# Kernel tuning notes

Measured on AMD Instinct MI355X. Metric: run time of the kernel, lower is better.

The kernel has to match this reference:

```python
import jax, jax.numpy as jnp
import numpy as np

B, S, I, E, D = 64, 512, 64, 256, 256  # batch, src_len, input_size, enc_hid, dec_hid


def _lstm_cell(h, c, x, Wih, Whh, b):
    # PyTorch LSTM gate order: i, f, g, o ; b = b_ih + b_hh combined
    z = x @ Wih.T + h @ Whh.T + b
    i, f, g, o = jnp.split(z, 4, axis=-1)
    c = jax.nn.sigmoid(f) * c + jax.nn.sigmoid(i) * jnp.tanh(g)
    h = jax.nn.sigmoid(o) * jnp.tanh(c)
    return h, c


def _run_lstm(x, h0, c0, Wih, Whh, b):
    # x: [B,S,I] -> outputs [B,S,H]
    def step(carry, xt):
        h, c = _lstm_cell(carry[0], carry[1], xt, Wih, Whh, b)
        return (h, c), h
    _, ys = jax.lax.scan(step, (h0, c0), jnp.swapaxes(x, 0, 1))
    return jnp.swapaxes(ys, 0, 1)


def _forward(x, enc_h0, enc_c0, dec_h0, dec_c0, Wih_f, Whh_f, b_f, Wih_b, Whh_b, b_b,
             W_attn, b_attn, v, Wih_d, Whh_d, b_d, W_lin, b_lin):
    b_, s_ = x.shape[0], x.shape[1]
    # bidirectional encoder
    out_f = _run_lstm(x, enc_h0[0], enc_c0[0], Wih_f, Whh_f, b_f)
    out_b = _run_lstm(x[:, ::-1, :], enc_h0[1], enc_c0[1], Wih_b, Whh_b, b_b)[:, ::-1, :]
    enc_out = jnp.concatenate([out_f, out_b], axis=-1)  # [B,S,2E]
    h0d, c0d = dec_h0[0], dec_c0[0]  # decoder re-starts from these EVERY step (faithful)

    @jax.checkpoint
    def dec_step(carry, _):
        y, h_attn = carry  # y: [B,1], h_attn: [B,D]
        dh = h_attn.shape[-1]
        cat = jnp.concatenate(
            [jnp.broadcast_to(h_attn[:, None, :], (b_, s_, dh)), enc_out], axis=-1)
        energy = jnp.tanh(cat @ W_attn.T + b_attn)              # [B,S,D]
        attn = jax.nn.softmax(jnp.einsum('d,bsd->bs', v, energy), axis=1)
        context = jnp.einsum('bs,bse->be', attn, enc_out)       # [B,2E]
        dec_in = jnp.concatenate([y, context], axis=-1)         # [B,1+2E]
        h_new, _c = _lstm_cell(h0d, c0d, dec_in, Wih_d, Whh_d, b_d)
        y_new = jnp.concatenate([h_new, context], axis=-1) @ W_lin.T + b_lin  # [B,1]
        return (y_new, h_new), y_new

    y0 = jnp.zeros((b_, 1), dtype=x.dtype)
    _, ys = jax.lax.scan(dec_step, (y0, h0d), None, length=s_)  # [S,B,1]
    # output_size == 1, so torch's cat-then-[:,1:] equals the stacked per-step ys
    return jnp.swapaxes(ys, 0, 1).reshape(b_, s_)


def setup_inputs() -> dict:
    key = jax.random.key(0)
    ks = jax.random.split(key, 20)
    W = 0.05  # weight scale ~ torch default init magnitude
    rn = lambda k, sh, s: jax.random.normal(k, sh, dtype=jnp.float32) * s
    return {
        'x': rn(ks[0], (B, S, I), 1.0),
        'enc_h0': rn(ks[1], (2, B, E), 1.0),
        'enc_c0': rn(ks[2], (2, B, E), 1.0),
        'dec_h0': rn(ks[3], (1, B, D), 1.0),
        'dec_c0': rn(ks[4], (1, B, D), 1.0),
        'Wih_f': rn(ks[5], (4 * E, I), W),
        'Whh_f': rn(ks[6], (4 * E, E), W),
        'b_f': rn(ks[7], (4 * E,), W),
        'Wih_b': rn(ks[8], (4 * E, I), W),
        'Whh_b': rn(ks[9], (4 * E, E), W),
        'b_b': rn(ks[10], (4 * E,), W),
        'W_attn': rn(ks[11], (D, D + 2 * E), W),
        'b_attn': rn(ks[12], (D,), W),
        'v': jax.random.uniform(ks[13], (D,), dtype=jnp.float32),
        'Wih_d': rn(ks[14], (4 * D, 2 * E + 1), W),
        'Whh_d': rn(ks[15], (4 * D, D), W),
        'b_d': rn(ks[16], (4 * D,), W),
        'W_lin': rn(ks[17], (1, 2 * E + D), W),
        'b_lin': rn(ks[18], (1,), W),
    }


def reference(x, enc_h0, enc_c0, dec_h0, dec_c0, Wih_f, Whh_f, b_f, Wih_b, Whh_b, b_b,
              W_attn, b_attn, v, Wih_d, Whh_d, b_d, W_lin, b_lin):
    return _forward(x, enc_h0, enc_c0, dec_h0, dec_c0, Wih_f, Whh_f, b_f,
                    Wih_b, Whh_b, b_b, W_attn, b_attn, v, Wih_d, Whh_d, b_d,
                    W_lin, b_lin)
```

## Files before the change

### kernel.cpp

```cpp
#include <hip/hip_runtime.h>
#include <hip/hip_bf16.h>

#define NB 64
#define NS 512
#define NI 64
#define NE 256
#define ND 256
#define N4E 1024
#define N4D 1024
#define NTE 512
#define G 4
#define SLICE 128
#define CELLS 64

__device__ __forceinline__ float fsig(float x){
    return __fdividef(1.f, 1.f + __expf(-x));
}
__device__ __forceinline__ float ftanh(float x){
    x = fminf(10.f, fmaxf(-10.f, x));
    float e = __expf(2.f*x);
    return 1.f - __fdividef(2.f, e + 1.f);
}
__device__ __forceinline__ float wave_sum(float v){
    #pragma unroll
    for (int o=32;o>0;o>>=1) v += __shfl_xor(v, o, 64);
    return v;
}
__device__ __forceinline__ float wave_max(float v){
    #pragma unroll
    for (int o=32;o>0;o>>=1) v = fmaxf(v, __shfl_xor(v, o, 64));
    return v;
}
__device__ __forceinline__ float blo(unsigned u){ return __uint_as_float(u<<16); }
__device__ __forceinline__ float bhi(unsigned u){ return __uint_as_float(u & 0xffff0000u); }
__device__ __forceinline__ unsigned short bfbits(float f){
    __hip_bfloat16 h = __float2bfloat16(f);
    return *(unsigned short*)&h;
}
__device__ __forceinline__ float ld_agf(const float* p){
    return __hip_atomic_load(p, __ATOMIC_RELAXED, __HIP_MEMORY_SCOPE_AGENT);
}
__device__ __forceinline__ void st_agf(float* p, float v){
    __hip_atomic_store(p, v, __ATOMIC_RELAXED, __HIP_MEMORY_SCOPE_AGENT);
}

__device__ __forceinline__ void groupbar(unsigned* c, unsigned tgt, int tid){
    __syncthreads();
    if (tid == 0){
        __hip_atomic_fetch_add(c, 1u, __ATOMIC_RELAXED, __HIP_MEMORY_SCOPE_AGENT);
        while (__hip_atomic_load(c, __ATOMIC_RELAXED, __HIP_MEMORY_SCOPE_AGENT) < tgt)
            __builtin_amdgcn_s_sleep(2);
    }
    __syncthreads();
}

__global__ void k_transpose(float* __restrict__ dst, const float* __restrict__ src,
                            int R, int C, int ld, int off){
    int idx = blockIdx.x*256 + threadIdx.x;
    if (idx >= R*C) return;
    int r = idx / C, c = idx - r*C;
    dst[(size_t)c*R + r] = src[(size_t)r*ld + off + c];
}
__global__ void k_transpose16(__hip_bfloat16* __restrict__ dst, const float* __restrict__ src,
                              int R, int C, int ld, int off){
    int idx = blockIdx.x*256 + threadIdx.x;
    if (idx >= R*C) return;
    int r = idx / C, c = idx - r*C;
    dst[(size_t)c*R + r] = __float2bfloat16(src[(size_t)r*ld + off + c]);
}

__global__ void k_pack_wy(float* __restrict__ wy, const float* __restrict__ Wih_d){
    int j = blockIdx.x*256 + threadIdx.x;
    if (j < N4D) wy[j] = Wih_d[(size_t)j*(NTE+1)];
}

__global__ void k_pack_wdtg(__hip_bfloat16* __restrict__ dst, const float* __restrict__ Wih_d){
    int idx = blockIdx.x*256 + threadIdx.x;
    int q = idx >> 17, rem = idx & 131071;
    int e = rem >> 8, jj = rem & 255;
    int j = ((jj>>6)<<8) + (q<<6) + (jj&63);
    dst[idx] = __float2bfloat16(Wih_d[(size_t)j*(NTE+1) + 1 + e]);
}

__global__ void k_zc(float* __restrict__ zc, const float* __restrict__ WhhTd,
                     const float* __restrict__ h0d, const float* __restrict__ b_d){
    int b = blockIdx.x, tid = threadIdx.x;
    __shared__ float h0[ND];
    if (tid < ND) h0[tid] = h0d[b*ND + tid];
    __syncthreads();
    for (int j = tid; j < N4D; j += 256){
        float acc = b_d[j];
        #pragma unroll 8
        for (int d=0; d<ND; ++d) acc = fmaf(h0[d], WhhTd[d*N4D + j], acc);
        zc[b*N4D + j] = acc;
    }
}

__global__ void k_dec_init(float* __restrict__ hG, float* __restrict__ yG,
                           unsigned* __restrict__ ctr, const float* __restrict__ dec_h0){
    int b = blockIdx.x, tid = threadIdx.x;
    hG[b*ND + tid] = dec_h0[b*ND + tid];
    if (tid < G) yG[b*G + tid] = 0.f;
    if (tid == 0) ctr[b] = 0u;
}

__global__ __launch_bounds__(512) void k_enc(
    const float* __restrict__ x, const float* __restrict__ eh0, const float* __restrict__ ec0,
    const __hip_bfloat16* __restrict__ WihTf, const __hip_bfloat16* __restrict__ WhhTf, const float* __restrict__ bf,
    const __hip_bfloat16* __restrict__ WihTb, const __hip_bfloat16* __restrict__ WhhTb, const float* __restrict__ bb,
    __hip_bfloat16* __restrict__ eo16)
{
    int bid = blockIdx.x;
    int dir = bid & 1, b = bid >> 1;
    const unsigned* Wih2 = (const unsigned*)(dir ? WihTb : WihTf);
    const unsigned* Whh2 = (const unsigned*)(dir ? WhhTb : WhhTf);
    const float*  bias = dir ? bb : bf;
    int tid = threadIdx.x;
    __shared__ float h[NE], c[NE], xt[NI], z[N4E];
    __shared__ float2 bl[512];
    bl[tid] = ((const float2*)bias)[tid];
    if (tid < NE){
        h[tid] = eh0[(dir*NB + b)*NE + tid];
        c[tid] = ec0[(dir*NB + b)*NE + tid];
    }
    __syncthreads();
    for (int t=0; t<NS; ++t){
        int st = dir ? (NS-1-t) : t;
        if (tid < NI) xt[tid] = x[((size_t)b*NS + st)*NI + tid];
        __syncthreads();
        float2 acc = bl[tid];
        #pragma unroll 8
        for (int i=0;i<NI;++i){
            float xv = xt[i]; unsigned w = Wih2[i*512 + tid];
            acc.x = fmaf(xv, blo(w), acc.x); acc.y = fmaf(xv, bhi(w), acc.y);
        }
        #pragma unroll 8
        for (int d=0;d<NE;++d){
            float hv = h[d]; unsigned w = Whh2[d*512 + tid];
            acc.x = fmaf(hv, blo(w), acc.x); acc.y = fmaf(hv, bhi(w), acc.y);
        }
        ((float2*)z)[tid] = acc;
        __syncthreads();
        if (tid < NE){
            float zi=z[tid], zf=z[NE+tid], zg=z[2*NE+tid], zo=z[3*NE+tid];
            float cn = fsig(zf)*c[tid] + fsig(zi)*ftanh(zg);
            float hn = fsig(zo)*ftanh(cn);
            c[tid]=cn; h[tid]=hn;
            eo16[((size_t)b*NS + st)*NTE + dir*NE + tid] = __float2bfloat16(hn);
        }
        __syncthreads();
    }
}

__global__ __launch_bounds__(256) void k_encproj(const unsigned* __restrict__ eo32,
        const float* __restrict__ WeT, const float* __restrict__ b_attn,
        unsigned short* __restrict__ ep_pk16){
    int b = blockIdx.y, s0 = blockIdx.x*16, tid = threadIdx.x;
    __shared__ float tile[16*NTE];
    {
        const unsigned* eop = eo32 + (size_t)(b*NS + s0)*256;
        for (int k=0;k<32;++k){
            int wi = k*256 + tid;
            unsigned w = eop[wi];
            int sl = wi>>8, ew = wi&255;
            tile[sl*NTE + 2*ew]   = blo(w);
            tile[sl*NTE + 2*ew+1] = bhi(w);
        }
    }
    __syncthreads();
    float acc[16];
    float ba = b_attn[tid];
    #pragma unroll
    for (int sl=0;sl<16;++sl) acc[sl]=ba;
    #pragma unroll 4
    for (int e4=0;e4<128;++e4){
        float w0 = WeT[(4*e4+0)*ND+tid];
        float w1 = WeT[(4*e4+1)*ND+tid];
        float w2 = WeT[(4*e4+2)*ND+tid];
        float w3 = WeT[(4*e4+3)*ND+tid];
        #pragma unroll
        for (int sl=0;sl<16;++sl){
            const float4 tv = *(const float4*)&tile[sl*NTE + 4*e4];
            acc[sl] = fmaf(tv.x,w0,fmaf(tv.y,w1,fmaf(tv.z,w2,fmaf(tv.w,w3,acc[sl]))));
        }
    }
    #pragma unroll
    for (int sl=0;sl<16;++sl){
        int s = s0+sl;
        size_t wdi = ((size_t)(b*4 + (s>>7))*128 + (tid>>1))*128 + (s&127);
        ep_pk16[wdi*2 + (tid&1)] = bfbits(acc[sl]);
    }
}

__global__ __launch_bounds__(1024, 4) void k_dec(
    const unsigned* __restrict__ eo32,
    const unsigned* __restrict__ ep_pk,
    const unsigned* __restrict__ WhTp,
    const float* __restrict__ v,
    const float* __restrict__ zc, const float* __restrict__ wy,
    const unsigned* __restrict__ WdTp_all,
    const float* __restrict__ dec_c0,
    const float* __restrict__ W_lin, const float* __restrict__ b_lin,
    float* __restrict__ hG, float* __restrict__ yG,
    float* __restrict__ ctxG, float* __restrict__ msG,
    unsigned* __restrict__ ctr,
    float* __restrict__ out)
{
    int bid = blockIdx.x;
    int b = bid & 63, q = bid >> 6;
    int tid = threadIdx.x;

    __shared__ unsigned ep_lds[16384];
    __shared__ float part[2048];
    __shared__ float h_l[ND];
    __shared__ float2 hv[ND];
    __shared__ float v_l[ND];
    __shared__ float scores_l[SLICE];
    __shared__ float ctx_l[NTE];
    __shared__ float z_l[256], zc_l[256], wy_l[256];
    __shared__ float c0_l[CELLS], wlh_l[CELLS], wlc_l[SLICE];
    __shared__ float msbuf[8];
    __shared__ float wred[16];
    __shared__ float smax, yprev;

    const unsigned* WdTp = WdTp_all + (size_t)q*NTE*128;

    for (int i=tid; i<16384; i+=1024)
        ep_lds[i] = ep_pk[(size_t)(b*4+q)*16384 + i];
    unsigned eo_reg[32];
    {
        int ep2 = tid & 255, sq = tid >> 8;
        const unsigned* eop = eo32 + (size_t)(b*NS + q*SLICE + sq*32)*256 + ep2;
        #pragma unroll
        for (int ss=0; ss<32; ++ss) eo_reg[ss] = eop[(size_t)ss*256];
    }
    if (tid < 256){
        int jj = tid;
        int j = ((jj>>6)<<8) + (q<<6) + (jj&63);
        zc_l[jj] = zc[b*N4D + j];
        wy_l[jj] = wy[j];
        v_l[tid] = v[tid];
    }
    if (tid < CELLS){
        c0_l[tid]  = dec_c0[b*ND + q*CELLS + tid];
        wlh_l[tid] = W_lin[q*CELLS + tid];
    }
    if (tid < SLICE) wlc_l[tid] = W_lin[ND + q*SLICE + tid];
    float blin = b_lin[0];
    __syncthreads();

    for (int t=0; t<NS; ++t){
        if (tid < ND) h_l[tid] = ld_agf(&hG[b*ND + tid]);
        if (tid == 0){
            float y = 0.f;
            if (t > 0){
                y = blin + ld_agf(&yG[b*G+0]) + ld_agf(&yG[b*G+1])
                         + ld_agf(&yG[b*G+2]) + ld_agf(&yG[b*G+3]);
                if (q == 0) out[(size_t)b*NS + (t-1)] = y;
            }
            yprev = y;
        }
        __syncthreads();
        {
            int d2 = tid & 127, kq = tid >> 7;
            float ax = 0.f, ay = 0.f;
            #pragma unroll 8
            for (int kk=0; kk<32; ++kk){
                int k = kq*32 + kk;
                unsigned w = WhTp[k*128 + d2];
                float hvv = h_l[k];
                ax = fmaf(hvv, blo(w), ax); ay = fmaf(hvv, bhi(w), ay);
            }
            ((float2*)part)[kq*128 + d2] = make_float2(ax, ay);
        }
        __syncthreads();
        if (tid < ND){
            float s = 0.f;
            #pragma unroll
            for (int r=0;r<8;++r) s += part[r*256 + tid];
            hv[tid] = make_float2(v_l[tid], s);
        }
        __syncthreads();
        {
            int sl = tid & 127, dg = tid >> 7;
            float sc = 0.f;
            const unsigned* epl = ep_lds + dg*16*128 + sl;
            #pragma unroll
            for (int k16=0; k16<16; ++k16){
                unsigned w = epl[k16*128];
                int d = dg*32 + 2*k16;
                float2 a0 = hv[d], a1 = hv[d+1];
                sc += a0.x*ftanh(blo(w) + a0.y) + a1.x*ftanh(bhi(w) + a1.y);
            }
            part[dg*128 + sl] = sc;
        }
        __syncthreads();
        if (tid < SLICE){
            float s = 0.f;
            #pragma unroll
            for (int r=0;r<8;++r) s += part[r*128 + tid];
            part[1024 + tid] = s;
            float wm = wave_max(s);
            if ((tid&63)==0) wred[tid>>6] = wm;
        }
        __syncthreads();
        if (tid == 0) smax = fmaxf(wred[0], wred[1]);
        __syncthreads();
        if (tid < SLICE){
            float ev = __expf(part[1024 + tid] - smax);
            scores_l[tid] = ev;
            float s = wave_sum(ev);
            if ((tid&63)==0) wred[2+(tid>>6)] = s;
        }
        __syncthreads();
        if (tid == 0){
            st_agf(&msG[(b*G+q)*2+0], smax);
            st_agf(&msG[(b*G+q)*2+1], wred[2]+wred[3]);
        }
        {
            int ep2 = tid & 255, sq = tid >> 8;
            float ax = 0.f, ay = 0.f;
            #pragma unroll
            for (int ss=0; ss<32; ++ss){
                unsigned w = eo_reg[ss];
                float sc = scores_l[sq*32 + ss];
                ax = fmaf(sc, blo(w), ax); ay = fmaf(sc, bhi(w), ay);
            }
            ((float2*)part)[sq*256 + ep2] = make_float2(ax, ay);
        }
        __syncthreads();
        if (tid < NTE){
            float s = part[tid] + part[512+tid] + part[1024+tid] + part[1536+tid];
            st_agf(&ctxG[(size_t)(b*G+q)*NTE + tid], s);
        }
        groupbar(&ctr[b], (unsigned)(t*2*G + G), tid);
        if (tid < 2*G) msbuf[tid] = ld_agf(&msG[b*G*2 + tid]);
        __syncthreads();
        float mm = fmaxf(fmaxf(msbuf[0], msbuf[2]), fmaxf(msbuf[4], msbuf[6]));
        float w0 = __expf(msbuf[0]-mm), w1 = __expf(msbuf[2]-mm),
              w2 = __expf(msbuf[4]-mm), w3 = __expf(msbuf[6]-mm);
        float inv = __fdividef(1.f, msbuf[1]*w0 + msbuf[3]*w1 + msbuf[5]*w2 + msbuf[7]*w3);
        if (tid < NTE){
            const float* cg = ctxG + (size_t)b*G*NTE + tid;
            float cacc = ld_agf(cg)*w0 + ld_agf(cg+NTE)*w1
                       + ld_agf(cg+2*NTE)*w2 + ld_agf(cg+3*NTE)*w3;
            ctx_l[tid] = cacc * inv;
        }
        __syncthreads();
        {
            int jj2 = tid & 127, eq = tid >> 7;
            float ax = 0.f, ay = 0.f;
            #pragma unroll 8
            for (int ee=0; ee<64; ++ee){
                int e = eq*64 + ee;
                unsigned w = WdTp[e*128 + jj2];
                float cv = ctx_l[e];
                ax = fmaf(cv, blo(w), ax); ay = fmaf(cv, bhi(w), ay);
            }
            ((float2*)part)[eq*128 + jj2] = make_float2(ax, ay);
        }
        __syncthreads();
        if (tid < 256){
            float s = zc_l[tid] + yprev*wy_l[tid];
            #pragma unroll
            for (int r=0;r<8;++r) s += part[r*256 + tid];
            z_l[tid] = s;
        }
        __syncthreads();
        float yp = 0.f;
        if (tid < CELLS){
            float zi=z_l[tid], zf=z_l[64+tid], zg=z_l[128+tid], zo=z_l[192+tid];
            float cn = fsig(zf)*c0_l[tid] + fsig(zi)*ftanh(zg);
            float hn = fsig(zo)*ftanh(cn);
            st_agf(&hG[b*ND + q*CELLS + tid], hn);
            yp = hn * wlh_l[tid];
        } else if (tid < CELLS + SLICE){
            yp = ctx_l[q*SLICE + (tid - CELLS)] * wlc_l[tid - CELLS];
        }
        {
            float s = wave_sum(yp);
            if ((tid&63)==0 && tid < 192) wred[8+(tid>>6)] = s;
        }
        __syncthreads();
        if (tid == 0) st_agf(&yG[b*G + q], wred[8]+wred[9]+wred[10]);
        groupbar(&ctr[b], (unsigned)(t*2*G + 2*G), tid);
    }
    if (q == 0 && tid == 0){
        out[(size_t)b*NS + (NS-1)] = blin + ld_agf(&yG[b*G+0]) + ld_agf(&yG[b*G+1])
                                          + ld_agf(&yG[b*G+2]) + ld_agf(&yG[b*G+3]);
    }
}

extern "C" void kernel_launch(void* const* d_in, const int* in_sizes, int n_in,
                              void* d_out, int out_size, void* d_ws, size_t ws_size,
                              hipStream_t stream){
    const float* x      = (const float*)d_in[0];
    const float* enc_h0 = (const float*)d_in[1];
    const float* enc_c0 = (const float*)d_in[2];
    const float* dec_h0 = (const float*)d_in[3];
    const float* dec_c0 = (const float*)d_in[4];
    const float* Wih_f  = (const float*)d_in[5];
    const float* Whh_f  = (const float*)d_in[6];
    const float* b_f    = (const float*)d_in[7];
    const float* Wih_b  = (const float*)d_in[8];
    const float* Whh_b  = (const float*)d_in[9];
    const float* b_b    = (const float*)d_in[10];
    const float* W_attn = (const float*)d_in[11];
    const float* b_attn = (const float*)d_in[12];
    const float* v      = (const float*)d_in[13];
    const float* Wih_d  = (const float*)d_in[14];
    const float* Whh_d  = (const float*)d_in[15];
    const float* b_d    = (const float*)d_in[16];
    const float* W_lin  = (const float*)d_in[17];
    const float* b_lin  = (const float*)d_in[18];
    float* out = (float*)d_out;
    char* ws   = (char*)d_ws;

    size_t off = 0;
    auto alloc = [&](size_t bytes)->size_t{ size_t o = off; off += (bytes + 255) & ~(size_t)255; return o; };
    size_t o_eo16   = alloc((size_t)NB*NS*NTE*2);
    size_t o_eppk   = alloc((size_t)NB*G*128*128*4);
    size_t o_WihTf  = alloc((size_t)NI*N4E*2);
    size_t o_WhhTf  = alloc((size_t)NE*N4E*2);
    size_t o_WihTb  = alloc((size_t)NI*N4E*2);
    size_t o_WhhTb  = alloc((size_t)NE*N4E*2);
    size_t o_WhT16  = alloc((size_t)ND*ND*2);
    size_t o_WeT    = alloc((size_t)NTE*ND*4);
    size_t o_WdTg   = alloc((size_t)G*NTE*256*2);
    size_t o_WhhTd  = alloc((size_t)ND*N4D*4);
    size_t o_zc     = alloc((size_t)NB*N4D*4);
    size_t o_wy     = alloc((size_t)N4D*4);
    size_t o_hG     = alloc((size_t)NB*ND*4);
    size_t o_yG     = alloc((size_t)NB*G*4);
    size_t o_ctxG   = alloc((size_t)NB*G*NTE*4);
    size_t o_msG    = alloc((size_t)NB*G*2*4);
    size_t o_ctr    = alloc((size_t)NB*4);
    if (ws_size < off) return;

    auto F   = [&](size_t o)->float*{ return (float*)(ws + o); };
    auto U32 = [&](size_t o)->unsigned*{ return (unsigned*)(ws + o); };
    auto H16 = [&](size_t o)->__hip_bfloat16*{ return (__hip_bfloat16*)(ws + o); };

    auto T32 = [&](size_t dsto, const float* src, int R, int C, int ld, int offc){
        int n = R*C;
        k_transpose<<<dim3((n+255)/256), dim3(256), 0, stream>>>(F(dsto), src, R, C, ld, offc);
    };
    auto T16 = [&](size_t dsto, const float* src, int R, int C, int ld, int offc){
        int n = R*C;
        k_transpose16<<<dim3((n+255)/256), dim3(256), 0, stream>>>(H16(dsto), src, R, C, ld, offc);
    };
    T16(o_WihTf, Wih_f, N4E, NI, NI, 0);
    T16(o_WhhTf, Whh_f, N4E, NE, NE, 0);
    T16(o_WihTb, Wih_b, N4E, NI, NI, 0);
    T16(o_WhhTb, Whh_b, N4E, NE, NE, 0);
    T16(o_WhT16, W_attn, ND, ND, ND+NTE, 0);
    T32(o_WeT,   W_attn, ND, NTE, ND+NTE, ND);
    T32(o_WhhTd, Whh_d, N4D, ND, ND, 0);
    k_pack_wdtg<<<dim3((G*NTE*256)/256), dim3(256), 0, stream>>>(H16(o_WdTg), Wih_d);
    k_pack_wy<<<dim3(4), dim3(256), 0, stream>>>(F(o_wy), Wih_d);
    k_zc<<<dim3(NB), dim3(256), 0, stream>>>(F(o_zc), F(o_WhhTd), dec_h0, b_d);
    k_dec_init<<<dim3(NB), dim3(256), 0, stream>>>(F(o_hG), F(o_yG), (unsigned*)(ws+o_ctr), dec_h0);

    k_enc<<<dim3(2*NB), dim3(512), 0, stream>>>(x, enc_h0, enc_c0,
        H16(o_WihTf), H16(o_WhhTf), b_f, H16(o_WihTb), H16(o_WhhTb), b_b, H16(o_eo16));

    k_encproj<<<dim3(NS/16, NB), dim3(256), 0, stream>>>(U32(o_eo16), F(o_WeT), b_attn,
        (unsigned short*)(ws+o_eppk));

    k_dec<<<dim3(NB*G), dim3(1024), 0, stream>>>(U32(o_eo16), U32(o_eppk),
        U32(o_WhT16), v, F(o_zc), F(o_wy), U32(o_WdTg), dec_c0, W_lin, b_lin,
        F(o_hG), F(o_yG), F(o_ctxG), F(o_msG), (unsigned*)(ws+o_ctr), out);
}
```

Before: 19.51 ms.

## Restructure encoder LSTM to one gate row per thread with packed bf16 weights

Rewrites the encoder LSTM kernel to use 1024 threads per block, one gate row per thread, with row-major bf16-pair packed weights read as uint4. The input-to-hidden weights are held in registers, the x rows are double-buffered and prefetched for the next step, and the cell state stays in registers. Each step loses one barrier and the loads become wide per-row loads instead of strided column reads. In exchange there is more register pressure, and each thread now streams a 512-byte weight row per step whose loads are uncoalesced across the threads of a wave.

```diff
diff --git a/kernel.cpp b/kernel.cpp
--- a/kernel.cpp
+++ b/kernel.cpp
@@ -69,6 +69,15 @@
     dst[(size_t)c*R + r] = __float2bfloat16(src[(size_t)r*ld + off + c]);
 }
 
+__global__ void k_pack_pairs(unsigned* __restrict__ dst, const float* __restrict__ src,
+                             int n, int Cp){
+    int idx = blockIdx.x*256 + threadIdx.x;
+    if (idx >= n) return;
+    int r = idx / Cp, k = idx - r*Cp;
+    const float* s = src + (size_t)r*2*Cp + 2*k;
+    dst[idx] = (unsigned)bfbits(s[0]) | ((unsigned)bfbits(s[1])<<16);
+}
+
 __global__ void k_pack_wy(float* __restrict__ wy, const float* __restrict__ Wih_d){
     int j = blockIdx.x*256 + threadIdx.x;
     if (j < N4D) wy[j] = Wih_d[(size_t)j*(NTE+1)];
@@ -104,49 +113,91 @@
     if (tid == 0) ctr[b] = 0u;
 }
 
-__global__ __launch_bounds__(512) void k_enc(
+__global__ __launch_bounds__(1024, 4) void k_enc(
     const float* __restrict__ x, const float* __restrict__ eh0, const float* __restrict__ ec0,
-    const __hip_bfloat16* __restrict__ WihTf, const __hip_bfloat16* __restrict__ WhhTf, const float* __restrict__ bf,
-    const __hip_bfloat16* __restrict__ WihTb, const __hip_bfloat16* __restrict__ WhhTb, const float* __restrict__ bb,
-    __hip_bfloat16* __restrict__ eo16)
+    const unsigned* __restrict__ whhPKf, const unsigned* __restrict__ wihPKf, const float* __restrict__ bf,
+    const unsigned* __restrict__ whhPKb, const unsigned* __restrict__ wihPKb, const float* __restrict__ bb,
+    unsigned* __restrict__ eo32)
 {
     int bid = blockIdx.x;
-    int dir = bid & 1, b = bid >> 1;
-    const unsigned* Wih2 = (const unsigned*)(dir ? WihTb : WihTf);
-    const unsigned* Whh2 = (const unsigned*)(dir ? WhhTb : WhhTf);
-    const float*  bias = dir ? bb : bf;
+    int b = bid & 63, dir = bid >> 6;
     int tid = threadIdx.x;
-    __shared__ float h[NE], c[NE], xt[NI], z[N4E];
-    __shared__ float2 bl[512];
-    bl[tid] = ((const float2*)bias)[tid];
-    if (tid < NE){
-        h[tid] = eh0[(dir*NB + b)*NE + tid];
-        c[tid] = ec0[(dir*NB + b)*NE + tid];
+    const unsigned* whhPK = dir ? whhPKb : whhPKf;
+    const unsigned* wihPK = dir ? wihPKb : wihPKf;
+    const float* bias = dir ? bb : bf;
+
+    __shared__ __align__(16) float h_l[NE];
+    __shared__ __align__(16) float xt[2][NI];
+    __shared__ float z_l[N4E];
+
+    unsigned wih_r[32];
+    {
+        const uint4* wr = (const uint4*)(wihPK + (size_t)tid*32);
+        #pragma unroll
+        for (int k=0;k<8;++k) ((uint4*)wih_r)[k] = wr[k];
+    }
+    const uint4* wrow = (const uint4*)(whhPK + (size_t)tid*128);
+    float bias_r = bias[tid];
+
+    float c0r=0.f, c1r=0.f;
+    if (tid < 128){
+        h_l[2*tid]   = eh0[(dir*NB+b)*NE + 2*tid];
+        h_l[2*tid+1] = eh0[(dir*NB+b)*NE + 2*tid+1];
+        c0r = ec0[(dir*NB+b)*NE + 2*tid];
+        c1r = ec0[(dir*NB+b)*NE + 2*tid+1];
+    }
+    {
+        int st0 = dir ? (NS-1) : 0;
+        if (tid < 16) ((float4*)xt[0])[tid] = ((const float4*)(x + ((size_t)b*NS+st0)*NI))[tid];
     }
     __syncthreads();
-    for (int t=0; t<NS; ++t){
+
+    for (int t=0;t<NS;++t){
         int st = dir ? (NS-1-t) : t;
-        if (tid < NI) xt[tid] = x[((size_t)b*NS + st)*NI + tid];
-        __syncthreads();
-        float2 acc = bl[tid];
-        #pragma unroll 8
-        for (int i=0;i<NI;++i){
-            float xv = xt[i]; unsigned w = Wih2[i*512 + tid];
-            acc.x = fmaf(xv, blo(w), acc.x); acc.y = fmaf(xv, bhi(w), acc.y);
-        }
-        #pragma unroll 8
-        for (int d=0;d<NE;++d){
-            float hv = h[d]; unsigned w = Whh2[d*512 + tid];
-            acc.x = fmaf(hv, blo(w), acc.x); acc.y = fmaf(hv, bhi(w), acc.y);
-        }
-        ((float2*)z)[tid] = acc;
-        __syncthreads();
-        if (tid < NE){
-            float zi=z[tid], zf=z[NE+tid], zg=z[2*NE+tid], zo=z[3*NE+tid];
-            float cn = fsig(zf)*c[tid] + fsig(zi)*ftanh(zg);
-            float hn = fsig(zo)*ftanh(cn);
-            c[tid]=cn; h[tid]=hn;
-            eo16[((size_t)b*NS + st)*NTE + dir*NE + tid] = __float2bfloat16(hn);
+        float4 xpre = make_float4(0.f,0.f,0.f,0.f);
+        if (t+1 < NS && tid < 16){
+            int stn = dir ? (NS-2-t) : (t+1);
+            xpre = ((const float4*)(x + ((size_t)b*NS+stn)*NI))[tid];
+        }
+        const float* xc = xt[t&1];
+        float a0=bias_r, a1=0.f, a2=0.f, a3=0.f;
+        #pragma unroll
+        for (int k=0;k<16;++k){
+            float4 xv = ((const float4*)xc)[k];
+            unsigned w0 = wih_r[2*k], w1 = wih_r[2*k+1];
+            a0 = fmaf(xv.x, blo(w0), a0);
+            a1 = fmaf(xv.y, bhi(w0), a1);
+            a2 = fmaf(xv.z, blo(w1), a2);
+            a3 = fmaf(xv.w, bhi(w1), a3);
+        }
+        const float4* h4 = (const float4*)h_l;
+        #pragma unroll
+        for (int kk=0;kk<32;++kk){
+            uint4 w = wrow[kk];
+            float4 ha = h4[2*kk], hb = h4[2*kk+1];
+            a0 = fmaf(ha.x, blo(w.x), a0);
+            a1 = fmaf(ha.y, bhi(w.x), a1);
+            a2 = fmaf(ha.z, blo(w.y), a2);
+            a3 = fmaf(ha.w, bhi(w.y), a3);
+            a0 = fmaf(hb.x, blo(w.z), a0);
+            a1 = fmaf(hb.y, bhi(w.z), a1);
+            a2 = fmaf(hb.z, blo(w.w), a2);
+            a3 = fmaf(hb.w, bhi(w.w), a3);
+        }
+        z_l[tid] = (a0+a1)+(a2+a3);
+        if (t+1 < NS && tid < 16) ((float4*)xt[(t+1)&1])[tid] = xpre;
+        __syncthreads();
+        if (tid < 128){
+            int d0 = 2*tid, d1 = 2*tid+1;
+            float zi0=z_l[d0], zf0=z_l[NE+d0], zg0=z_l[2*NE+d0], zo0=z_l[3*NE+d0];
+            float zi1=z_l[d1], zf1=z_l[NE+d1], zg1=z_l[2*NE+d1], zo1=z_l[3*NE+d1];
+            c0r = fsig(zf0)*c0r + fsig(zi0)*ftanh(zg0);
+            c1r = fsig(zf1)*c1r + fsig(zi1)*ftanh(zg1);
+            float h0 = fsig(zo0)*ftanh(c0r);
+            float h1 = fsig(zo1)*ftanh(c1r);
+            h_l[d0]=h0; h_l[d1]=h1;
+            eo32[((size_t)b*NS+st)*(NTE/2) + dir*(NE/2) + tid] =
+                (unsigned)bfbits(h0) | ((unsigned)bfbits(h1)<<16);
         }
         __syncthreads();
     }
@@ -420,10 +471,10 @@
     auto alloc = [&](size_t bytes)->size_t{ size_t o = off; off += (bytes + 255) & ~(size_t)255; return o; };
     size_t o_eo16   = alloc((size_t)NB*NS*NTE*2);
     size_t o_eppk   = alloc((size_t)NB*G*128*128*4);
-    size_t o_WihTf  = alloc((size_t)NI*N4E*2);
-    size_t o_WhhTf  = alloc((size_t)NE*N4E*2);
-    size_t o_WihTb  = alloc((size_t)NI*N4E*2);
-    size_t o_WhhTb  = alloc((size_t)NE*N4E*2);
+    size_t o_whhPKf = alloc((size_t)N4E*128*4);
+    size_t o_whhPKb = alloc((size_t)N4E*128*4);
+    size_t o_wihPKf = alloc((size_t)N4E*32*4);
+    size_t o_wihPKb = alloc((size_t)N4E*32*4);
     size_t o_WhT16  = alloc((size_t)ND*ND*2);
     size_t o_WeT    = alloc((size_t)NTE*ND*4);
     size_t o_WdTg   = alloc((size_t)G*NTE*256*2);
@@ -449,10 +500,14 @@
         int n = R*C;
         k_transpose16<<<dim3((n+255)/256), dim3(256), 0, stream>>>(H16(dsto), src, R, C, ld, offc);
     };
-    T16(o_WihTf, Wih_f, N4E, NI, NI, 0);
-    T16(o_WhhTf, Whh_f, N4E, NE, NE, 0);
-    T16(o_WihTb, Wih_b, N4E, NI, NI, 0);
-    T16(o_WhhTb, Whh_b, N4E, NE, NE, 0);
+    auto PK = [&](size_t dsto, const float* src, int R, int Cp){
+        int n = R*Cp;
+        k_pack_pairs<<<dim3((n+255)/256), dim3(256), 0, stream>>>(U32(dsto), src, n, Cp);
+    };
+    PK(o_whhPKf, Whh_f, N4E, 128);
+    PK(o_whhPKb, Whh_b, N4E, 128);
+    PK(o_wihPKf, Wih_f, N4E, 32);
+    PK(o_wihPKb, Wih_b, N4E, 32);
     T16(o_WhT16, W_attn, ND, ND, ND+NTE, 0);
     T32(o_WeT,   W_attn, ND, NTE, ND+NTE, ND);
     T32(o_WhhTd, Whh_d, N4D, ND, ND, 0);
@@ -461,8 +516,8 @@
     k_zc<<<dim3(NB), dim3(256), 0, stream>>>(F(o_zc), F(o_WhhTd), dec_h0, b_d);
     k_dec_init<<<dim3(NB), dim3(256), 0, stream>>>(F(o_hG), F(o_yG), (unsigned*)(ws+o_ctr), dec_h0);
 
-    k_enc<<<dim3(2*NB), dim3(512), 0, stream>>>(x, enc_h0, enc_c0,
-        H16(o_WihTf), H16(o_WhhTf), b_f, H16(o_WihTb), H16(o_WhhTb), b_b, H16(o_eo16));
+    k_enc<<<dim3(2*NB), dim3(1024), 0, stream>>>(x, enc_h0, enc_c0,
+        U32(o_whhPKf), U32(o_wihPKf), b_f, U32(o_whhPKb), U32(o_wihPKb), b_b, U32(o_eo16));
 
     k_encproj<<<dim3(NS/16, NB), dim3(256), 0, stream>>>(U32(o_eo16), F(o_WeT), b_attn,
         (unsigned short*)(ws+o_eppk));
```

New measurement: 41.18 ms. 111% more time.

## Split encoder LSTM reduction across 1024 threads and use per-block flag barriers

Applied to the files above, without the earlier changes.

The encoder LSTM kernel now runs 1024 threads per block. It splits the input and hidden reductions across two halves that write partial gate sums, keeps the cell state in registers, and prefetches the next timestep's input into a double buffer. The decoder's counter-based group barrier becomes per-block monotonic flags polled by four threads, avoiding atomic read-modify-write contention. Context partial loads are issued before the __syncthreads to overlap latency. The changes aim to shorten the serial per-step latency of both recurrences, at the cost of an extra partial-sum reduction and more threads per block.

```diff
diff --git a/kernel.cpp b/kernel.cpp
--- a/kernel.cpp
+++ b/kernel.cpp
@@ -44,12 +44,15 @@
     __hip_atomic_store(p, v, __ATOMIC_RELAXED, __HIP_MEMORY_SCOPE_AGENT);
 }
 
-__device__ __forceinline__ void groupbar(unsigned* c, unsigned tgt, int tid){
+__device__ __forceinline__ void groupbar(unsigned* flags, int b, int q,
+                                         unsigned tgt, int tid){
     __syncthreads();
-    if (tid == 0){
-        __hip_atomic_fetch_add(c, 1u, __ATOMIC_RELAXED, __HIP_MEMORY_SCOPE_AGENT);
-        while (__hip_atomic_load(c, __ATOMIC_RELAXED, __HIP_MEMORY_SCOPE_AGENT) < tgt)
-            __builtin_amdgcn_s_sleep(2);
+    if (tid == 0)
+        __hip_atomic_store(&flags[b*4+q], tgt, __ATOMIC_RELAXED, __HIP_MEMORY_SCOPE_AGENT);
+    if (tid < 4){
+        while (__hip_atomic_load(&flags[b*4+tid], __ATOMIC_RELAXED,
+                                 __HIP_MEMORY_SCOPE_AGENT) < tgt)
+            __builtin_amdgcn_s_sleep(1);
     }
     __syncthreads();
 }
@@ -97,56 +100,89 @@
 }
 
 __global__ void k_dec_init(float* __restrict__ hG, float* __restrict__ yG,
-                           unsigned* __restrict__ ctr, const float* __restrict__ dec_h0){
+                           unsigned* __restrict__ flags, const float* __restrict__ dec_h0){
     int b = blockIdx.x, tid = threadIdx.x;
     hG[b*ND + tid] = dec_h0[b*ND + tid];
     if (tid < G) yG[b*G + tid] = 0.f;
-    if (tid == 0) ctr[b] = 0u;
-}
-
-__global__ __launch_bounds__(512) void k_enc(
+    if (tid < G) flags[b*G + tid] = 0u;
+}
+
+__global__ __launch_bounds__(1024) void k_enc(
     const float* __restrict__ x, const float* __restrict__ eh0, const float* __restrict__ ec0,
-    const __hip_bfloat16* __restrict__ WihTf, const __hip_bfloat16* __restrict__ WhhTf, const float* __restrict__ bf,
-    const __hip_bfloat16* __restrict__ WihTb, const __hip_bfloat16* __restrict__ WhhTb, const float* __restrict__ bb,
-    __hip_bfloat16* __restrict__ eo16)
+    const unsigned* __restrict__ whhTf, const unsigned* __restrict__ wihTf, const float* __restrict__ bf,
+    const unsigned* __restrict__ whhTb, const unsigned* __restrict__ wihTb, const float* __restrict__ bb,
+    unsigned* __restrict__ eo32)
 {
     int bid = blockIdx.x;
-    int dir = bid & 1, b = bid >> 1;
-    const unsigned* Wih2 = (const unsigned*)(dir ? WihTb : WihTf);
-    const unsigned* Whh2 = (const unsigned*)(dir ? WhhTb : WhhTf);
-    const float*  bias = dir ? bb : bf;
+    int b = bid & 63, dir = bid >> 6;
     int tid = threadIdx.x;
-    __shared__ float h[NE], c[NE], xt[NI], z[N4E];
-    __shared__ float2 bl[512];
-    bl[tid] = ((const float2*)bias)[tid];
+    int j2 = tid & 511, kh = tid >> 9;
+    const unsigned* whh = dir ? whhTb : whhTf;
+    const unsigned* wih = dir ? wihTb : wihTf;
+    const float* bias = dir ? bb : bf;
+
+    __shared__ __align__(16) float h_l[NE];
+    __shared__ __align__(16) float xt[2][NI];
+    __shared__ float zp0[N4E], zp1[N4E];
+
+    float2 bias2 = make_float2(0.f, 0.f);
+    if (kh == 0) bias2 = ((const float2*)bias)[j2];
+
+    float cst = 0.f;
     if (tid < NE){
-        h[tid] = eh0[(dir*NB + b)*NE + tid];
-        c[tid] = ec0[(dir*NB + b)*NE + tid];
+        h_l[tid] = eh0[(dir*NB+b)*NE + tid];
+        cst      = ec0[(dir*NB+b)*NE + tid];
+    }
+    {
+        int st0 = dir ? (NS-1) : 0;
+        if (tid < 16) ((float4*)xt[0])[tid] = ((const float4*)(x + ((size_t)b*NS+st0)*NI))[tid];
     }
     __syncthreads();
-    for (int t=0; t<NS; ++t){
+
+    const unsigned* wihK = wih + (size_t)(kh*32)*512 + j2;
+    const unsigned* whhK = whh + (size_t)(kh*128)*512 + j2;
+    float* zpme = kh ? zp1 : zp0;
+
+    for (int t=0;t<NS;++t){
         int st = dir ? (NS-1-t) : t;
-        if (tid < NI) xt[tid] = x[((size_t)b*NS + st)*NI + tid];
-        __syncthreads();
-        float2 acc = bl[tid];
+        float4 xpre = make_float4(0.f,0.f,0.f,0.f);
+        if (t+1 < NS && tid < 16){
+            int stn = dir ? (NS-2-t) : (t+1);
+            xpre = ((const float4*)(x + ((size_t)b*NS+stn)*NI))[tid];
+        }
+        const float* xc = xt[t&1];
+        float x0=bias2.x, y0=bias2.y, x1=0.f, y1=0.f;
         #pragma unroll 8
-        for (int i=0;i<NI;++i){
-            float xv = xt[i]; unsigned w = Wih2[i*512 + tid];
-            acc.x = fmaf(xv, blo(w), acc.x); acc.y = fmaf(xv, bhi(w), acc.y);
+        for (int ii=0; ii<32; ii+=2){
+            int i = kh*32 + ii;
+            unsigned wa = wihK[(size_t)ii*512];
+            unsigned wb = wihK[(size_t)(ii+1)*512];
+            float xa = xc[i], xb = xc[i+1];
+            x0 = fmaf(xa, blo(wa), x0); y0 = fmaf(xa, bhi(wa), y0);
+            x1 = fmaf(xb, blo(wb), x1); y1 = fmaf(xb, bhi(wb), y1);
         }
         #pragma unroll 8
-        for (int d=0;d<NE;++d){
-            float hv = h[d]; unsigned w = Whh2[d*512 + tid];
-            acc.x = fmaf(hv, blo(w), acc.x); acc.y = fmaf(hv, bhi(w), acc.y);
-        }
-        ((float2*)z)[tid] = acc;
+        for (int dd=0; dd<128; dd+=2){
+            int d = kh*128 + dd;
+            unsigned wa = whhK[(size_t)dd*512];
+            unsigned wb = whhK[(size_t)(dd+1)*512];
+            float ha = h_l[d], hb = h_l[d+1];
+            x0 = fmaf(ha, blo(wa), x0); y0 = fmaf(ha, bhi(wa), y0);
+            x1 = fmaf(hb, blo(wb), x1); y1 = fmaf(hb, bhi(wb), y1);
+        }
+        ((float2*)zpme)[j2] = make_float2(x0+x1, y0+y1);
+        if (t+1 < NS && tid < 16) ((float4*)xt[(t+1)&1])[tid] = xpre;
         __syncthreads();
         if (tid < NE){
-            float zi=z[tid], zf=z[NE+tid], zg=z[2*NE+tid], zo=z[3*NE+tid];
-            float cn = fsig(zf)*c[tid] + fsig(zi)*ftanh(zg);
-            float hn = fsig(zo)*ftanh(cn);
-            c[tid]=cn; h[tid]=hn;
-            eo16[((size_t)b*NS + st)*NTE + dir*NE + tid] = __float2bfloat16(hn);
+            int c = tid;
+            float zi = zp0[c]        + zp1[c];
+            float zf = zp0[NE+c]     + zp1[NE+c];
+            float zg = zp0[2*NE+c]   + zp1[2*NE+c];
+            float zo = zp0[3*NE+c]   + zp1[3*NE+c];
+            cst = fsig(zf)*cst + fsig(zi)*ftanh(zg);
+            float hn = fsig(zo)*ftanh(cst);
+            h_l[c] = hn;
+            ((unsigned short*)eo32)[((size_t)b*NS+st)*NTE + dir*NE + c] = bfbits(hn);
         }
         __syncthreads();
     }
@@ -203,7 +239,7 @@
     const float* __restrict__ W_lin, const float* __restrict__ b_lin,
     float* __restrict__ hG, float* __restrict__ yG,
     float* __restrict__ ctxG, float* __restrict__ msG,
-    unsigned* __restrict__ ctr,
+    unsigned* __restrict__ flags,
     float* __restrict__ out)
 {
     int bid = blockIdx.x;
@@ -333,19 +369,21 @@
             float s = part[tid] + part[512+tid] + part[1024+tid] + part[1536+tid];
             st_agf(&ctxG[(size_t)(b*G+q)*NTE + tid], s);
         }
-        groupbar(&ctr[b], (unsigned)(t*2*G + G), tid);
+        groupbar(flags, b, q, (unsigned)(2*t+1), tid);
+        float cg0=0.f, cg1=0.f, cg2=0.f, cg3=0.f;
         if (tid < 2*G) msbuf[tid] = ld_agf(&msG[b*G*2 + tid]);
+        if (tid < NTE){
+            const float* cg = ctxG + (size_t)b*G*NTE + tid;
+            cg0 = ld_agf(cg);        cg1 = ld_agf(cg+NTE);
+            cg2 = ld_agf(cg+2*NTE);  cg3 = ld_agf(cg+3*NTE);
+        }
         __syncthreads();
         float mm = fmaxf(fmaxf(msbuf[0], msbuf[2]), fmaxf(msbuf[4], msbuf[6]));
         float w0 = __expf(msbuf[0]-mm), w1 = __expf(msbuf[2]-mm),
               w2 = __expf(msbuf[4]-mm), w3 = __expf(msbuf[6]-mm);
         float inv = __fdividef(1.f, msbuf[1]*w0 + msbuf[3]*w1 + msbuf[5]*w2 + msbuf[7]*w3);
-        if (tid < NTE){
-            const float* cg = ctxG + (size_t)b*G*NTE + tid;
-            float cacc = ld_agf(cg)*w0 + ld_agf(cg+NTE)*w1
-                       + ld_agf(cg+2*NTE)*w2 + ld_agf(cg+3*NTE)*w3;
-            ctx_l[tid] = cacc * inv;
-        }
+        if (tid < NTE)
+            ctx_l[tid] = (cg0*w0 + cg1*w1 + cg2*w2 + cg3*w3) * inv;
         __syncthreads();
         {
             int jj2 = tid & 127, eq = tid >> 7;
@@ -383,7 +421,7 @@
         }
         __syncthreads();
         if (tid == 0) st_agf(&yG[b*G + q], wred[8]+wred[9]+wred[10]);
-        groupbar(&ctr[b], (unsigned)(t*2*G + 2*G), tid);
+        groupbar(flags, b, q, (unsigned)(2*t+2), tid);
     }
     if (q == 0 && tid == 0){
         out[(size_t)b*NS + (NS-1)] = blin + ld_agf(&yG[b*G+0]) + ld_agf(&yG[b*G+1])
@@ -434,7 +472,7 @@
     size_t o_yG     = alloc((size_t)NB*G*4);
     size_t o_ctxG   = alloc((size_t)NB*G*NTE*4);
     size_t o_msG    = alloc((size_t)NB*G*2*4);
-    size_t o_ctr    = alloc((size_t)NB*4);
+    size_t o_flags  = alloc((size_t)NB*G*4);
     if (ws_size < off) return;
 
     auto F   = [&](size_t o)->float*{ return (float*)(ws + o); };
@@ -459,15 +497,15 @@
     k_pack_wdtg<<<dim3((G*NTE*256)/256), dim3(256), 0, stream>>>(H16(o_WdTg), Wih_d);
     k_pack_wy<<<dim3(4), dim3(256), 0, stream>>>(F(o_wy), Wih_d);
     k_zc<<<dim3(NB), dim3(256), 0, stream>>>(F(o_zc), F(o_WhhTd), dec_h0, b_d);
-    k_dec_init<<<dim3(NB), dim3(256), 0, stream>>>(F(o_hG), F(o_yG), (unsigned*)(ws+o_ctr), dec_h0);
-
-    k_enc<<<dim3(2*NB), dim3(512), 0, stream>>>(x, enc_h0, enc_c0,
-        H16(o_WihTf), H16(o_WhhTf), b_f, H16(o_WihTb), H16(o_WhhTb), b_b, H16(o_eo16));
+    k_dec_init<<<dim3(NB), dim3(256), 0, stream>>>(F(o_hG), F(o_yG), (unsigned*)(ws+o_flags), dec_h0);
+
+    k_enc<<<dim3(2*NB), dim3(1024), 0, stream>>>(x, enc_h0, enc_c0,
+        U32(o_WhhTf), U32(o_WihTf), b_f, U32(o_WhhTb), U32(o_WihTb), b_b, U32(o_eo16));
 
     k_encproj<<<dim3(NS/16, NB), dim3(256), 0, stream>>>(U32(o_eo16), F(o_WeT), b_attn,
         (unsigned short*)(ws+o_eppk));
 
     k_dec<<<dim3(NB*G), dim3(1024), 0, stream>>>(U32(o_eo16), U32(o_eppk),
         U32(o_WhT16), v, F(o_zc), F(o_wy), U32(o_WdTg), dec_c0, W_lin, b_lin,
-        F(o_hG), F(o_yG), F(o_ctxG), F(o_msG), (unsigned*)(ws+o_ctr), out);
-}
+        F(o_hG), F(o_yG), F(o_ctxG), F(o_msG), (unsigned*)(ws+o_flags), out);
+}
```

Result: faster. 18.35 ms (-6.0%).
